# Optimization experiments

Measured on AMD Instinct MI355X. Metric: run time of the kernel, lower is better.

Reference implementation:

```python
import jax, jax.numpy as jnp
import numpy as np

B, N, F0 = 256, 256, 128
LAYER_SIZES = [128, 128, 128]


def setup_inputs() -> dict:
    key = jax.random.key(0)
    ks = jax.random.split(key, 10)
    x = jax.random.normal(ks[0], (B, N, F0), dtype=jnp.float32)
    adj = jax.random.uniform(ks[1], (B, N, N), dtype=jnp.float32)
    adj = 0.5 * (adj + jnp.swapaxes(adj, -1, -2))  # symmetric weighted adjacency
    f0, f1, f2 = LAYER_SIZES
    W1 = jax.random.normal(ks[2], (f0, f1), dtype=jnp.float32) / np.sqrt(f0)
    b1 = jnp.zeros((f1,), dtype=jnp.float32)
    W2 = jax.random.normal(ks[3], (f1, f2), dtype=jnp.float32) / np.sqrt(f1)
    b2 = jnp.zeros((f2,), dtype=jnp.float32)
    Wr = jax.random.normal(ks[4], (2 * f2, f2), dtype=jnp.float32) / np.sqrt(2 * f2)
    br = jnp.zeros((f2,), dtype=jnp.float32)
    return {"x": x, "adj": adj, "W1": W1, "b1": b1, "W2": W2, "b2": b2, "Wr": Wr, "br": br}


def _normalize_adj(adj):
    # DenseGCNConv: set self-loops (diag=1), then D^{-1/2} (A+I) D^{-1/2} with deg clamped to >=1
    n = adj.shape[-1]
    eye = jnp.eye(n, dtype=adj.dtype)
    a = adj * (1.0 - eye) + eye
    d = jnp.maximum(a.sum(axis=-1), 1.0) ** -0.5  # [B, N]
    return d[..., :, None] * a * d[..., None, :]


def reference(x, adj, W1, b1, W2, b2, Wr, br):
    a = _normalize_adj(adj)  # same adj for both layers; normalization is identical per layer
    h = jnp.einsum("bnm,bmf->bnf", a, x @ W1) + b1  # DenseGCNConv layer 1
    h = jnp.einsum("bnm,bmf->bnf", a, h @ W2) + b2  # DenseGCNConv layer 2
    pooled = jnp.concatenate([h.mean(axis=1), h.max(axis=1)], axis=-1)  # [B, 2F]
    return pooled @ Wr + br  # [B, F]
```

## Files before the change

kernel.cpp:

```cpp
#include <hip/hip_runtime.h>
#include <cstddef>


typedef __attribute__((ext_vector_type(8))) short short8;
typedef __attribute__((ext_vector_type(4))) float f32x4;

static __device__ __forceinline__ unsigned short f2bf(float f) {
  unsigned int u = __float_as_uint(f);
  u += 0x7FFFu + ((u >> 16) & 1u);
  return (unsigned short)(u >> 16);
}

static __device__ __forceinline__ f32x4 mfma16(short8 a, short8 b, f32x4 c) {
  return __builtin_amdgcn_mfma_f32_16x16x32_bf16(a, b, c, 0, 0, 0);
}

static __device__ __forceinline__ int byteT(int f, int k) {
  return ((f << 9) + (k << 1)) ^ ((f & 7) << 4);
}
static __device__ __forceinline__ int byteH(int n, int k) {
  return ((n << 8) + (k << 1)) ^ ((n & 7) << 4);
}

static __device__ __forceinline__ void p0_load(float4 (&v)[8],
    const float* __restrict__ adjb, int rbase, int c0) {
  #pragma unroll
  for (int i = 0; i < 8; ++i)
    v[i] = *reinterpret_cast<const float4*>(adjb + ((rbase + i) << 8) + c0);
}
static __device__ __forceinline__ void p0_proc(float4 (&v)[8],
    unsigned short* __restrict__ Abw, int rbase, int c0,
    float& sx, float& sy, float& sz, float& sw) {
  #pragma unroll
  for (int i = 0; i < 8; ++i) {
    const int r = rbase + i;
    v[i].x = (r == c0 + 0) ? 1.0f : v[i].x;
    v[i].y = (r == c0 + 1) ? 1.0f : v[i].y;
    v[i].z = (r == c0 + 2) ? 1.0f : v[i].z;
    v[i].w = (r == c0 + 3) ? 1.0f : v[i].w;
    sx += v[i].x; sy += v[i].y; sz += v[i].z; sw += v[i].w;
    ushort4 o;
    o.x = f2bf(v[i].x); o.y = f2bf(v[i].y);
    o.z = f2bf(v[i].z); o.w = f2bf(v[i].w);
    *reinterpret_cast<ushort4*>(Abw + (r << 8) + c0) = o;
  }
}

__global__ __launch_bounds__(64) void k_packW2(
    const float* __restrict__ W1, const float* __restrict__ W2,
    unsigned short* __restrict__ P1, unsigned short* __restrict__ P2) {
  const float* W = (blockIdx.x < 32) ? W1 : W2;
  unsigned short* P = (blockIdx.x < 32) ? P1 : P2;
  const int bb = blockIdx.x & 31;
  const int ks = bb >> 3;
  const int r = bb & 7;
  const int l = threadIdx.x;
  const int col = r * 16 + (l & 15);
  const int k0 = ks * 32 + ((l >> 4) << 3);
  short8 frag;
  #pragma unroll
  for (int j = 0; j < 8; ++j)
    frag[j] = (short)f2bf(W[(size_t)(k0 + j) * 128 + col]);
  *reinterpret_cast<short8*>(P + ((size_t)((ks * 8 + r) * 64 + l)) * 8) = frag;
}

__global__ __launch_bounds__(512) void k_fused(
    const float* __restrict__ adj, const float* __restrict__ x,
    const unsigned short* __restrict__ W1p, const unsigned short* __restrict__ W2p,
    const float* __restrict__ b1, const float* __restrict__ b2,
    const float* __restrict__ Wr, const float* __restrict__ br,
    unsigned short* __restrict__ Abf, float* __restrict__ out) {
  __shared__ __align__(16) char bufA[65536];
  __shared__ __align__(16) char bufB[65536];
  __shared__ float dinv_s[256];

  const int b = blockIdx.x;
  const int tid = threadIdx.x;
  const int w = tid >> 6;
  const int l = tid & 63;
  const int l15 = l & 15;
  const int khalf = (l >> 4) << 3;
  const int qbase = (l >> 4) << 2;
  const int m = (w << 4) + l15;
  const unsigned short* Ab = Abf + ((size_t)b << 16);
  const int n0w = w << 5;

  float4 xa[4];
  {
    const float* xr = x + ((((size_t)b << 8) + m) << 7);
    #pragma unroll
    for (int k = 0; k < 2; ++k) {
      xa[2 * k]     = *reinterpret_cast<const float4*>(xr + (k << 5) + khalf);
      xa[2 * k + 1] = *reinterpret_cast<const float4*>(xr + (k << 5) + khalf + 4);
    }
  }

  {
    const int c0 = l << 2;
    const float* adjb = adj + ((size_t)b << 16);
    unsigned short* Abw = Abf + ((size_t)b << 16);
    float sx = 0.f, sy = 0.f, sz = 0.f, sw = 0.f;
    float4 va[8], vb[8];
    p0_load(va, adjb, n0w + 0, c0);
    p0_load(vb, adjb, n0w + 8, c0);
    p0_proc(va, Abw, n0w + 0, c0, sx, sy, sz, sw);
    p0_load(va, adjb, n0w + 16, c0);
    p0_proc(vb, Abw, n0w + 8, c0, sx, sy, sz, sw);
    p0_load(vb, adjb, n0w + 24, c0);
    p0_proc(va, Abw, n0w + 16, c0, sx, sy, sz, sw);
    p0_proc(vb, Abw, n0w + 24, c0, sx, sy, sz, sw);
    float* red = reinterpret_cast<float*>(bufA);
    float4 st; st.x = sx; st.y = sy; st.z = sz; st.w = sw;
    *reinterpret_cast<float4*>(red + (w << 8) + c0) = st;
  }
  __syncthreads();
  if (tid < 256) {
    const float* red = reinterpret_cast<const float*>(bufA);
    float s = 0.f;
    #pragma unroll
    for (int g = 0; g < 8; ++g) s += red[(g << 8) + tid];
    dinv_s[tid] = rsqrtf(fmaxf(s, 1.0f));
  }
  __syncthreads();

  {
    const short8* Wf = reinterpret_cast<const short8*>(W1p);
    {
      const float* xr = x + ((((size_t)b << 8) + m) << 7);
      float4 xb[4];
      #pragma unroll
      for (int ks = 2; ks < 4; ++ks) {
        xb[2 * (ks - 2)]     = *reinterpret_cast<const float4*>(xr + (ks << 5) + khalf);
        xb[2 * (ks - 2) + 1] = *reinterpret_cast<const float4*>(xr + (ks << 5) + khalf + 4);
      }
      f32x4 acc[8];
      #pragma unroll
      for (int r = 0; r < 8; ++r) acc[r] = (f32x4)(0.0f);
      #pragma unroll
      for (int ks = 0; ks < 4; ++ks) {
        const float4 u = (ks < 2) ? xa[2 * ks] : xb[2 * (ks - 2)];
        const float4 vv = (ks < 2) ? xa[2 * ks + 1] : xb[2 * (ks - 2) + 1];
        short8 bf;
        bf[0] = (short)f2bf(u.x);  bf[1] = (short)f2bf(u.y);
        bf[2] = (short)f2bf(u.z);  bf[3] = (short)f2bf(u.w);
        bf[4] = (short)f2bf(vv.x); bf[5] = (short)f2bf(vv.y);
        bf[6] = (short)f2bf(vv.z); bf[7] = (short)f2bf(vv.w);
        #pragma unroll
        for (int r = 0; r < 8; ++r)
          acc[r] = mfma16(Wf[((ks << 3) + r) * 64 + l], bf, acc[r]);
      }
      const float sc = dinv_s[m];
      #pragma unroll
      for (int r = 0; r < 8; ++r)
        #pragma unroll
        for (int q = 0; q < 4; ++q)
          *reinterpret_cast<unsigned short*>(bufA + byteT((r << 4) + qbase + q, m)) =
              f2bf(acc[r][q] * sc);
    }
    {
      const int m1 = m + 128;
      const float* xr = x + ((((size_t)b << 8) + m1) << 7);
      float4 xc[8];
      #pragma unroll
      for (int ks = 0; ks < 4; ++ks) {
        xc[2 * ks]     = *reinterpret_cast<const float4*>(xr + (ks << 5) + khalf);
        xc[2 * ks + 1] = *reinterpret_cast<const float4*>(xr + (ks << 5) + khalf + 4);
      }
      f32x4 acc[8];
      #pragma unroll
      for (int r = 0; r < 8; ++r) acc[r] = (f32x4)(0.0f);
      #pragma unroll
      for (int ks = 0; ks < 4; ++ks) {
        const float4 u = xc[2 * ks], vv = xc[2 * ks + 1];
        short8 bf;
        bf[0] = (short)f2bf(u.x);  bf[1] = (short)f2bf(u.y);
        bf[2] = (short)f2bf(u.z);  bf[3] = (short)f2bf(u.w);
        bf[4] = (short)f2bf(vv.x); bf[5] = (short)f2bf(vv.y);
        bf[6] = (short)f2bf(vv.z); bf[7] = (short)f2bf(vv.w);
        #pragma unroll
        for (int r = 0; r < 8; ++r)
          acc[r] = mfma16(Wf[((ks << 3) + r) * 64 + l], bf, acc[r]);
      }
      const float sc = dinv_s[m1];
      #pragma unroll
      for (int r = 0; r < 8; ++r)
        #pragma unroll
        for (int q = 0; q < 4; ++q)
          *reinterpret_cast<unsigned short*>(bufA + byteT((r << 4) + qbase + q, m1)) =
              f2bf(acc[r][q] * sc);
    }
  }
  __syncthreads();

  {
    float bs[8];
    #pragma unroll
    for (int c = 0; c < 8; ++c) bs[c] = b1[(c << 4) + l15];
    #pragma unroll
    for (int rt = 0; rt < 2; ++rt) {
      const int nb = n0w + (rt << 4);
      short8 af[8];
      #pragma unroll
      for (int ks = 0; ks < 8; ++ks)
        af[ks] = *reinterpret_cast<const short8*>(
            Ab + (size_t)(nb + l15) * 256 + (ks << 5) + khalf);
      f32x4 acc[8];
      #pragma unroll
      for (int c = 0; c < 8; ++c) acc[c] = (f32x4)(0.0f);
      #pragma unroll
      for (int ks = 0; ks < 8; ++ks) {
        const int k0 = (ks << 5) + khalf;
        #pragma unroll
        for (int c = 0; c < 8; ++c) {
          short8 bf = *reinterpret_cast<const short8*>(bufA + byteT((c << 4) + l15, k0));
          acc[c] = mfma16(af[ks], bf, acc[c]);
        }
      }
      #pragma unroll
      for (int q = 0; q < 4; ++q) {
        const int n = nb + qbase + q;
        const float dv = dinv_s[n];
        #pragma unroll
        for (int c = 0; c < 8; ++c)
          *reinterpret_cast<unsigned short*>(bufB + byteH(n, (c << 4) + l15)) =
              f2bf(acc[c][q] * dv + bs[c]);
      }
    }
  }
  __syncthreads();

  {
    const short8* Wf = reinterpret_cast<const short8*>(W2p);
    #pragma unroll
    for (int p = 0; p < 2; ++p) {
      const int mp = (p << 7) + m;
      f32x4 acc[8];
      #pragma unroll
      for (int r = 0; r < 8; ++r) acc[r] = (f32x4)(0.0f);
      #pragma unroll
      for (int ks = 0; ks < 4; ++ks) {
        const int kk = (ks << 5) + khalf;
        short8 hf = *reinterpret_cast<const short8*>(bufB + byteH(mp, kk));
        #pragma unroll
        for (int r = 0; r < 8; ++r)
          acc[r] = mfma16(Wf[((ks << 3) + r) * 64 + l], hf, acc[r]);
      }
      const float sc = dinv_s[mp];
      #pragma unroll
      for (int r = 0; r < 8; ++r)
        #pragma unroll
        for (int q = 0; q < 4; ++q)
          *reinterpret_cast<unsigned short*>(bufA + byteT((r << 4) + qbase + q, mp)) =
              f2bf(acc[r][q] * sc);
    }
  }
  __syncthreads();

  {
    float bs[8], psum[8], pmax[8];
    #pragma unroll
    for (int c = 0; c < 8; ++c) {
      bs[c] = b2[(c << 4) + l15];
      psum[c] = 0.0f; pmax[c] = -1e30f;
    }
    #pragma unroll
    for (int rt = 0; rt < 2; ++rt) {
      const int nb = n0w + (rt << 4);
      short8 af[8];
      #pragma unroll
      for (int ks = 0; ks < 8; ++ks)
        af[ks] = *reinterpret_cast<const short8*>(
            Ab + (size_t)(nb + l15) * 256 + (ks << 5) + khalf);
      f32x4 acc[8];
      #pragma unroll
      for (int c = 0; c < 8; ++c) acc[c] = (f32x4)(0.0f);
      #pragma unroll
      for (int ks = 0; ks < 8; ++ks) {
        const int k0 = (ks << 5) + khalf;
        #pragma unroll
        for (int c = 0; c < 8; ++c) {
          short8 bf = *reinterpret_cast<const short8*>(bufA + byteT((c << 4) + l15, k0));
          acc[c] = mfma16(af[ks], bf, acc[c]);
        }
      }
      #pragma unroll
      for (int q = 0; q < 4; ++q) {
        const int n = nb + qbase + q;
        const float dv = dinv_s[n];
        #pragma unroll
        for (int c = 0; c < 8; ++c) {
          const float v = acc[c][q] * dv + bs[c];
          psum[c] += v;
          pmax[c] = fmaxf(pmax[c], v);
        }
      }
    }
    #pragma unroll
    for (int c = 0; c < 8; ++c) {
      psum[c] += __shfl_xor(psum[c], 16);
      pmax[c] = fmaxf(pmax[c], __shfl_xor(pmax[c], 16));
      psum[c] += __shfl_xor(psum[c], 32);
      pmax[c] = fmaxf(pmax[c], __shfl_xor(pmax[c], 32));
    }
    float* lds_sum = reinterpret_cast<float*>(bufB);
    float* lds_max = lds_sum + 1024;
    float* pooled  = lds_max + 1024;
    float* rp      = pooled + 256;
    if (l < 16) {
      #pragma unroll
      for (int c = 0; c < 8; ++c) {
        lds_sum[(w << 7) + (c << 4) + l] = psum[c];
        lds_max[(w << 7) + (c << 4) + l] = pmax[c];
      }
    }
    __syncthreads();
    if (tid < 128) {
      float s = 0.0f;
      #pragma unroll
      for (int ww = 0; ww < 8; ++ww) s += lds_sum[(ww << 7) + tid];
      pooled[tid] = s * (1.0f / 256.0f);
    } else if (tid < 256) {
      const int f = tid & 127;
      float mx = -1e30f;
      #pragma unroll
      for (int ww = 0; ww < 8; ++ww) mx = fmaxf(mx, lds_max[(ww << 7) + f]);
      pooled[128 + f] = mx;
    }
    __syncthreads();
    {
      const int f = tid & 127, part = tid >> 7;
      const int base = part << 6;
      float o0 = 0.f, o1 = 0.f;
      #pragma unroll 4
      for (int i = 0; i < 64; i += 2) {
        o0 = fmaf(pooled[base + i],     Wr[(base + i) * 128 + f],     o0);
        o1 = fmaf(pooled[base + i + 1], Wr[(base + i + 1) * 128 + f], o1);
      }
      rp[(part << 7) + f] = o0 + o1;
    }
    __syncthreads();
    if (tid < 128) {
      out[(b << 7) + tid] =
          ((rp[tid] + rp[128 + tid]) + (rp[256 + tid] + rp[384 + tid])) + br[tid];
    }
  }
}

extern "C" void kernel_launch(void* const* d_in, const int* in_sizes, int n_in,
                              void* d_out, int out_size, void* d_ws, size_t ws_size,
                              hipStream_t stream) {
  const float* x   = (const float*)d_in[0];
  const float* adj = (const float*)d_in[1];
  const float* W1  = (const float*)d_in[2];
  const float* b1  = (const float*)d_in[3];
  const float* W2  = (const float*)d_in[4];
  const float* b2  = (const float*)d_in[5];
  const float* Wr  = (const float*)d_in[6];
  const float* br  = (const float*)d_in[7];
  float* out = (float*)d_out;

  char* ws = (char*)d_ws;
  unsigned short* Abf = (unsigned short*)(ws);
  unsigned short* W1p = (unsigned short*)(ws + 33554432);
  unsigned short* W2p = (unsigned short*)(ws + 33587200);

  k_packW2<<<64, 64, 0, stream>>>(W1, W2, W1p, W2p);
  k_fused<<<256, 512, 0, stream>>>(adj, x, W1p, W2p, b1, b2, Wr, br, Abf, out);
}
```

Before: 58.28 us.

## Read fp32 adjacency directly with register prefetch instead of bf16 workspace

Removes the bf16 copy of the patched adjacency that was written to global memory and reread in both aggregation layers. Each aggregation now rereads the fp32 adjacency rows, patches the diagonal and converts to bf16 in registers, prefetching the next half-row while MFMAs run. This eliminates the global write and its read-after-write dependency, but doubles the bytes read per aggregation and increases register pressure.

```diff
diff --git a/kernel.cpp b/kernel.cpp
--- a/kernel.cpp
+++ b/kernel.cpp
@@ -20,6 +20,33 @@
 }
 static __device__ __forceinline__ int byteH(int n, int k) {
   return ((n << 8) + (k << 1)) ^ ((n & 7) << 4);
+}
+
+static __device__ __forceinline__ short8 cvt_patch(float4 u, float4 v,
+                                                   int n, int k0) {
+  u.x = (n == k0 + 0) ? 1.0f : u.x;
+  u.y = (n == k0 + 1) ? 1.0f : u.y;
+  u.z = (n == k0 + 2) ? 1.0f : u.z;
+  u.w = (n == k0 + 3) ? 1.0f : u.w;
+  v.x = (n == k0 + 4) ? 1.0f : v.x;
+  v.y = (n == k0 + 5) ? 1.0f : v.y;
+  v.z = (n == k0 + 6) ? 1.0f : v.z;
+  v.w = (n == k0 + 7) ? 1.0f : v.w;
+  short8 f;
+  f[0] = (short)f2bf(u.x); f[1] = (short)f2bf(u.y);
+  f[2] = (short)f2bf(u.z); f[3] = (short)f2bf(u.w);
+  f[4] = (short)f2bf(v.x); f[5] = (short)f2bf(v.y);
+  f[6] = (short)f2bf(v.z); f[7] = (short)f2bf(v.w);
+  return f;
+}
+
+static __device__ __forceinline__ void ldfr(float4 (&g)[8],
+    const float* __restrict__ row, int khalf, int ksbase) {
+  #pragma unroll
+  for (int j = 0; j < 4; ++j) {
+    g[2 * j]     = *reinterpret_cast<const float4*>(row + ((ksbase + j) << 5) + khalf);
+    g[2 * j + 1] = *reinterpret_cast<const float4*>(row + ((ksbase + j) << 5) + khalf + 4);
+  }
 }
 
 static __device__ __forceinline__ void p0_load(float4 (&v)[8],
@@ -28,21 +55,15 @@
   for (int i = 0; i < 8; ++i)
     v[i] = *reinterpret_cast<const float4*>(adjb + ((rbase + i) << 8) + c0);
 }
-static __device__ __forceinline__ void p0_proc(float4 (&v)[8],
-    unsigned short* __restrict__ Abw, int rbase, int c0,
-    float& sx, float& sy, float& sz, float& sw) {
+static __device__ __forceinline__ void p0_acc(float4 (&v)[8],
+    int rbase, int c0, float& sx, float& sy, float& sz, float& sw) {
   #pragma unroll
   for (int i = 0; i < 8; ++i) {
     const int r = rbase + i;
-    v[i].x = (r == c0 + 0) ? 1.0f : v[i].x;
-    v[i].y = (r == c0 + 1) ? 1.0f : v[i].y;
-    v[i].z = (r == c0 + 2) ? 1.0f : v[i].z;
-    v[i].w = (r == c0 + 3) ? 1.0f : v[i].w;
-    sx += v[i].x; sy += v[i].y; sz += v[i].z; sw += v[i].w;
-    ushort4 o;
-    o.x = f2bf(v[i].x); o.y = f2bf(v[i].y);
-    o.z = f2bf(v[i].z); o.w = f2bf(v[i].w);
-    *reinterpret_cast<ushort4*>(Abw + (r << 8) + c0) = o;
+    sx += (r == c0 + 0) ? 1.0f : v[i].x;
+    sy += (r == c0 + 1) ? 1.0f : v[i].y;
+    sz += (r == c0 + 2) ? 1.0f : v[i].z;
+    sw += (r == c0 + 3) ? 1.0f : v[i].w;
   }
 }
 
@@ -69,7 +90,7 @@
     const unsigned short* __restrict__ W1p, const unsigned short* __restrict__ W2p,
     const float* __restrict__ b1, const float* __restrict__ b2,
     const float* __restrict__ Wr, const float* __restrict__ br,
-    unsigned short* __restrict__ Abf, float* __restrict__ out) {
+    float* __restrict__ out) {
   __shared__ __align__(16) char bufA[65536];
   __shared__ __align__(16) char bufB[65536];
   __shared__ float dinv_s[256];
@@ -82,8 +103,11 @@
   const int khalf = (l >> 4) << 3;
   const int qbase = (l >> 4) << 2;
   const int m = (w << 4) + l15;
-  const unsigned short* Ab = Abf + ((size_t)b << 16);
   const int n0w = w << 5;
+  const float* adjb = adj + ((size_t)b << 16);
+  const float* aRow0 = adjb + (size_t)(n0w + l15) * 256;
+
+  float4 ga[8];
 
   float4 xa[4];
   {
@@ -97,18 +121,16 @@
 
   {
     const int c0 = l << 2;
-    const float* adjb = adj + ((size_t)b << 16);
-    unsigned short* Abw = Abf + ((size_t)b << 16);
     float sx = 0.f, sy = 0.f, sz = 0.f, sw = 0.f;
     float4 va[8], vb[8];
     p0_load(va, adjb, n0w + 0, c0);
     p0_load(vb, adjb, n0w + 8, c0);
-    p0_proc(va, Abw, n0w + 0, c0, sx, sy, sz, sw);
+    p0_acc(va, n0w + 0, c0, sx, sy, sz, sw);
     p0_load(va, adjb, n0w + 16, c0);
-    p0_proc(vb, Abw, n0w + 8, c0, sx, sy, sz, sw);
+    p0_acc(vb, n0w + 8, c0, sx, sy, sz, sw);
     p0_load(vb, adjb, n0w + 24, c0);
-    p0_proc(va, Abw, n0w + 16, c0, sx, sy, sz, sw);
-    p0_proc(vb, Abw, n0w + 24, c0, sx, sy, sz, sw);
+    p0_acc(va, n0w + 16, c0, sx, sy, sz, sw);
+    p0_acc(vb, n0w + 24, c0, sx, sy, sz, sw);
     float* red = reinterpret_cast<float*>(bufA);
     float4 st; st.x = sx; st.y = sy; st.z = sz; st.w = sw;
     *reinterpret_cast<float4*>(red + (w << 8) + c0) = st;
@@ -189,6 +211,7 @@
           *reinterpret_cast<unsigned short*>(bufA + byteT((r << 4) + qbase + q, m1)) =
               f2bf(acc[r][q] * sc);
     }
+    ldfr(ga, aRow0, khalf, 0);
   }
   __syncthreads();
 
@@ -199,21 +222,37 @@
     #pragma unroll
     for (int rt = 0; rt < 2; ++rt) {
       const int nb = n0w + (rt << 4);
-      short8 af[8];
-      #pragma unroll
-      for (int ks = 0; ks < 8; ++ks)
-        af[ks] = *reinterpret_cast<const short8*>(
-            Ab + (size_t)(nb + l15) * 256 + (ks << 5) + khalf);
+      const int nl = nb + l15;
+      const float* arow = adjb + (size_t)nl * 256;
+      short8 afA[4], afB[4];
+      #pragma unroll
+      for (int j = 0; j < 4; ++j)
+        afA[j] = cvt_patch(ga[2 * j], ga[2 * j + 1], nl, (j << 5) + khalf);
+      ldfr(ga, arow, khalf, 4);
       f32x4 acc[8];
       #pragma unroll
       for (int c = 0; c < 8; ++c) acc[c] = (f32x4)(0.0f);
       #pragma unroll
-      for (int ks = 0; ks < 8; ++ks) {
+      for (int ks = 0; ks < 4; ++ks) {
         const int k0 = (ks << 5) + khalf;
         #pragma unroll
         for (int c = 0; c < 8; ++c) {
           short8 bf = *reinterpret_cast<const short8*>(bufA + byteT((c << 4) + l15, k0));
-          acc[c] = mfma16(af[ks], bf, acc[c]);
+          acc[c] = mfma16(afA[ks], bf, acc[c]);
+        }
+      }
+      #pragma unroll
+      for (int j = 0; j < 4; ++j)
+        afB[j] = cvt_patch(ga[2 * j], ga[2 * j + 1], nl, ((j + 4) << 5) + khalf);
+      if (rt == 0)
+        ldfr(ga, adjb + (size_t)(nl + 16) * 256, khalf, 0);
+      #pragma unroll
+      for (int ks = 4; ks < 8; ++ks) {
+        const int k0 = (ks << 5) + khalf;
+        #pragma unroll
+        for (int c = 0; c < 8; ++c) {
+          short8 bf = *reinterpret_cast<const short8*>(bufA + byteT((c << 4) + l15, k0));
+          acc[c] = mfma16(afB[ks - 4], bf, acc[c]);
         }
       }
       #pragma unroll
@@ -253,6 +292,7 @@
           *reinterpret_cast<unsigned short*>(bufA + byteT((r << 4) + qbase + q, mp)) =
               f2bf(acc[r][q] * sc);
     }
+    ldfr(ga, aRow0, khalf, 0);
   }
   __syncthreads();
 
@@ -266,21 +306,37 @@
     #pragma unroll
     for (int rt = 0; rt < 2; ++rt) {
       const int nb = n0w + (rt << 4);
-      short8 af[8];
-      #pragma unroll
-      for (int ks = 0; ks < 8; ++ks)
-        af[ks] = *reinterpret_cast<const short8*>(
-            Ab + (size_t)(nb + l15) * 256 + (ks << 5) + khalf);
+      const int nl = nb + l15;
+      const float* arow = adjb + (size_t)nl * 256;
+      short8 afA[4], afB[4];
+      #pragma unroll
+      for (int j = 0; j < 4; ++j)
+        afA[j] = cvt_patch(ga[2 * j], ga[2 * j + 1], nl, (j << 5) + khalf);
+      ldfr(ga, arow, khalf, 4);
       f32x4 acc[8];
       #pragma unroll
       for (int c = 0; c < 8; ++c) acc[c] = (f32x4)(0.0f);
       #pragma unroll
-      for (int ks = 0; ks < 8; ++ks) {
+      for (int ks = 0; ks < 4; ++ks) {
         const int k0 = (ks << 5) + khalf;
         #pragma unroll
         for (int c = 0; c < 8; ++c) {
           short8 bf = *reinterpret_cast<const short8*>(bufA + byteT((c << 4) + l15, k0));
-          acc[c] = mfma16(af[ks], bf, acc[c]);
+          acc[c] = mfma16(afA[ks], bf, acc[c]);
+        }
+      }
+      #pragma unroll
+      for (int j = 0; j < 4; ++j)
+        afB[j] = cvt_patch(ga[2 * j], ga[2 * j + 1], nl, ((j + 4) << 5) + khalf);
+      if (rt == 0)
+        ldfr(ga, adjb + (size_t)(nl + 16) * 256, khalf, 0);
+      #pragma unroll
+      for (int ks = 4; ks < 8; ++ks) {
+        const int k0 = (ks << 5) + khalf;
+        #pragma unroll
+        for (int c = 0; c < 8; ++c) {
+          short8 bf = *reinterpret_cast<const short8*>(bufA + byteT((c << 4) + l15, k0));
+          acc[c] = mfma16(afB[ks - 4], bf, acc[c]);
         }
       }
       #pragma unroll
@@ -360,10 +416,9 @@
   float* out = (float*)d_out;
 
   char* ws = (char*)d_ws;
-  unsigned short* Abf = (unsigned short*)(ws);
-  unsigned short* W1p = (unsigned short*)(ws + 33554432);
-  unsigned short* W2p = (unsigned short*)(ws + 33587200);
+  unsigned short* W1p = (unsigned short*)(ws);
+  unsigned short* W2p = (unsigned short*)(ws + 32768);
 
   k_packW2<<<64, 64, 0, stream>>>(W1, W2, W1p, W2p);
-  k_fused<<<256, 512, 0, stream>>>(adj, x, W1p, W2p, b1, b2, Wr, br, Abf, out);
-}
+  k_fused<<<256, 512, 0, stream>>>(adj, x, W1p, W2p, b1, b2, Wr, br, out);
+}
```

Result: slower. 113.9 us (+95.4%).

## Split adjacency degree and bf16 conversion into a separate wide kernel

Applied to the files above, without the earlier changes.

Moves the adjacency self-loop, row-degree and bf16 conversion pass out of the 256-block fused kernel into its own kernel with 2048 blocks. Each wave handles 8 rows and reduces degrees with shuffles, writing dinv to workspace. The fused kernel then only loads precomputed dinv. The aim is to use more of the GPU for the memory-bound 64MB adjacency read, since 256 blocks underfill the device. The cost is an extra launch and a round trip of dinv through global memory.

```diff
diff --git a/kernel.cpp b/kernel.cpp
--- a/kernel.cpp
+++ b/kernel.cpp
@@ -22,27 +22,47 @@
   return ((n << 8) + (k << 1)) ^ ((n & 7) << 4);
 }
 
-static __device__ __forceinline__ void p0_load(float4 (&v)[8],
-    const float* __restrict__ adjb, int rbase, int c0) {
-  #pragma unroll
-  for (int i = 0; i < 8; ++i)
-    v[i] = *reinterpret_cast<const float4*>(adjb + ((rbase + i) << 8) + c0);
-}
-static __device__ __forceinline__ void p0_proc(float4 (&v)[8],
-    unsigned short* __restrict__ Abw, int rbase, int c0,
-    float& sx, float& sy, float& sz, float& sw) {
-  #pragma unroll
-  for (int i = 0; i < 8; ++i) {
-    const int r = rbase + i;
-    v[i].x = (r == c0 + 0) ? 1.0f : v[i].x;
-    v[i].y = (r == c0 + 1) ? 1.0f : v[i].y;
-    v[i].z = (r == c0 + 2) ? 1.0f : v[i].z;
-    v[i].w = (r == c0 + 3) ? 1.0f : v[i].w;
-    sx += v[i].x; sy += v[i].y; sz += v[i].z; sw += v[i].w;
+__global__ __launch_bounds__(256) void k_deg_conv(
+    const float* __restrict__ adj, unsigned short* __restrict__ Abf,
+    float* __restrict__ dinv) {
+  const int wid = (blockIdx.x << 2) + (threadIdx.x >> 6);
+  const int t = threadIdx.x & 63;
+  const int row0 = wid << 3;
+  const size_t base0 = (size_t)row0 * 256;
+  const int c0 = 4 * t;
+
+  float4 v[8];
+  #pragma unroll
+  for (int r = 0; r < 8; ++r)
+    v[r] = *reinterpret_cast<const float4*>(adj + base0 + (size_t)r * 256 + c0);
+
+  float s[8];
+  #pragma unroll
+  for (int r = 0; r < 8; ++r) {
+    const int n = (row0 + r) & 255;
+    v[r].x = (n == c0 + 0) ? 1.0f : v[r].x;
+    v[r].y = (n == c0 + 1) ? 1.0f : v[r].y;
+    v[r].z = (n == c0 + 2) ? 1.0f : v[r].z;
+    v[r].w = (n == c0 + 3) ? 1.0f : v[r].w;
+    s[r] = (v[r].x + v[r].y) + (v[r].z + v[r].w);
+  }
+  #pragma unroll
+  for (int off = 32; off >= 1; off >>= 1) {
+    #pragma unroll
+    for (int r = 0; r < 8; ++r) s[r] += __shfl_xor(s[r], off);
+  }
+
+  float sel = s[0];
+  #pragma unroll
+  for (int r = 1; r < 8; ++r) sel = (t == r) ? s[r] : sel;
+  if (t < 8) dinv[row0 + t] = rsqrtf(fmaxf(sel, 1.0f));
+
+  #pragma unroll
+  for (int r = 0; r < 8; ++r) {
     ushort4 o;
-    o.x = f2bf(v[i].x); o.y = f2bf(v[i].y);
-    o.z = f2bf(v[i].z); o.w = f2bf(v[i].w);
-    *reinterpret_cast<ushort4*>(Abw + (r << 8) + c0) = o;
+    o.x = f2bf(v[r].x); o.y = f2bf(v[r].y);
+    o.z = f2bf(v[r].z); o.w = f2bf(v[r].w);
+    *reinterpret_cast<ushort4*>(Abf + base0 + (size_t)r * 256 + c0) = o;
   }
 }
 
@@ -65,11 +85,11 @@
 }
 
 __global__ __launch_bounds__(512) void k_fused(
-    const float* __restrict__ adj, const float* __restrict__ x,
+    const unsigned short* __restrict__ Abf, const float* __restrict__ x,
     const unsigned short* __restrict__ W1p, const unsigned short* __restrict__ W2p,
     const float* __restrict__ b1, const float* __restrict__ b2,
     const float* __restrict__ Wr, const float* __restrict__ br,
-    unsigned short* __restrict__ Abf, float* __restrict__ out) {
+    const float* __restrict__ dinv, float* __restrict__ out) {
   __shared__ __align__(16) char bufA[65536];
   __shared__ __align__(16) char bufB[65536];
   __shared__ float dinv_s[256];
@@ -94,33 +114,7 @@
       xa[2 * k + 1] = *reinterpret_cast<const float4*>(xr + (k << 5) + khalf + 4);
     }
   }
-
-  {
-    const int c0 = l << 2;
-    const float* adjb = adj + ((size_t)b << 16);
-    unsigned short* Abw = Abf + ((size_t)b << 16);
-    float sx = 0.f, sy = 0.f, sz = 0.f, sw = 0.f;
-    float4 va[8], vb[8];
-    p0_load(va, adjb, n0w + 0, c0);
-    p0_load(vb, adjb, n0w + 8, c0);
-    p0_proc(va, Abw, n0w + 0, c0, sx, sy, sz, sw);
-    p0_load(va, adjb, n0w + 16, c0);
-    p0_proc(vb, Abw, n0w + 8, c0, sx, sy, sz, sw);
-    p0_load(vb, adjb, n0w + 24, c0);
-    p0_proc(va, Abw, n0w + 16, c0, sx, sy, sz, sw);
-    p0_proc(vb, Abw, n0w + 24, c0, sx, sy, sz, sw);
-    float* red = reinterpret_cast<float*>(bufA);
-    float4 st; st.x = sx; st.y = sy; st.z = sz; st.w = sw;
-    *reinterpret_cast<float4*>(red + (w << 8) + c0) = st;
-  }
-  __syncthreads();
-  if (tid < 256) {
-    const float* red = reinterpret_cast<const float*>(bufA);
-    float s = 0.f;
-    #pragma unroll
-    for (int g = 0; g < 8; ++g) s += red[(g << 8) + tid];
-    dinv_s[tid] = rsqrtf(fmaxf(s, 1.0f));
-  }
+  if (tid < 256) dinv_s[tid] = dinv[(b << 8) + tid];
   __syncthreads();
 
   {
@@ -360,10 +354,12 @@
   float* out = (float*)d_out;
 
   char* ws = (char*)d_ws;
-  unsigned short* Abf = (unsigned short*)(ws);
-  unsigned short* W1p = (unsigned short*)(ws + 33554432);
-  unsigned short* W2p = (unsigned short*)(ws + 33587200);
+  unsigned short* Abf  = (unsigned short*)(ws);
+  float*          dinv = (float*)(ws + 33554432);
+  unsigned short* W1p  = (unsigned short*)(ws + 33816576);
+  unsigned short* W2p  = (unsigned short*)(ws + 33849344);
 
   k_packW2<<<64, 64, 0, stream>>>(W1, W2, W1p, W2p);
-  k_fused<<<256, 512, 0, stream>>>(adj, x, W1p, W2p, b1, b2, Wr, br, Abf, out);
-}
+  k_deg_conv<<<2048, 256, 0, stream>>>(adj, Abf, dinv);
+  k_fused<<<256, 512, 0, stream>>>(Abf, x, W1p, W2p, b1, b2, Wr, br, dinv, out);
+}
```

After: 63.58 us. 9.1% more time.
